# Performance work log

Hardware: AMD Instinct MI355X
Metric: run time of the kernel (lower is better)

Reference implementation:

```python
import jax, jax.numpy as jnp
import numpy as np

D_MODEL = 1024
N_HEAD = 16
D_HEAD = D_MODEL // N_HEAD
B, S = 4, 2048


def setup_inputs() -> dict:
    key = jax.random.key(0)
    ks = jax.random.split(key, 10)
    def xavier(k, shape):
        fan_in, fan_out = shape[1], shape[0]
        limit = np.sqrt(6.0 / (fan_in + fan_out))
        return jax.random.uniform(k, shape, jnp.float32, -limit, limit)
    x = jax.random.normal(ks[0], (B, S, D_MODEL), jnp.float32)
    mask = jnp.tril(jnp.ones((S, S), jnp.int32))[None, None]  # causal [1,1,S,S]
    return {
        "x": x,
        "Wq": xavier(ks[1], (D_MODEL, D_MODEL)), "bq": jnp.zeros((D_MODEL,), jnp.float32),
        "Wk": xavier(ks[2], (D_MODEL, D_MODEL)), "bk": jnp.zeros((D_MODEL,), jnp.float32),
        "Wv": xavier(ks[3], (D_MODEL, D_MODEL)), "bv": jnp.zeros((D_MODEL,), jnp.float32),
        "Wo": xavier(ks[4], (D_MODEL, D_MODEL)), "bo": jnp.zeros((D_MODEL,), jnp.float32),
        "mask": mask,
    }


def reference(x, Wq, bq, Wk, bk, Wv, bv, Wo, bo, mask):
    b, s, d = x.shape
    # Linear layers use y = x @ W.T + b (torch convention)
    def proj(W, bias):
        y = jnp.einsum('bsd,ed->bse', x, W) + bias
        return y.reshape(b, s, N_HEAD, D_HEAD).transpose(0, 2, 1, 3)  # [B,H,S,Dh]
    q = proj(Wq, bq)
    k = proj(Wk, bk)
    v = proj(Wv, bv)
    scores = jnp.einsum('bhqd,bhkd->bhqk', q, k) / jnp.sqrt(jnp.float32(D_HEAD))
    scores = jnp.where(mask == 0, jnp.float32(-1e9), scores)
    attn = jax.nn.softmax(scores, axis=-1)  # dropout is identity at eval
    context = jnp.einsum('bhqk,bhkd->bhqd', attn, v)
    context = context.transpose(0, 2, 1, 3).reshape(b, s, d)
    return jnp.einsum('bsd,ed->bse', context, Wo) + bo
```

## Files before the change

### kernel.cpp

```cpp
#include <hip/hip_runtime.h>
#include <stdint.h>

#define D_MODEL 1024
#define NHEAD   16
#define DHEAD   64
#define BATCH   4
#define SEQ     2048
#define MTOT    (BATCH*SEQ)

typedef __attribute__((ext_vector_type(4)))  float f32x4;
typedef __attribute__((ext_vector_type(8)))  short bf16x8;

typedef __attribute__((address_space(3))) uint32_t lds_u32;
typedef const __attribute__((address_space(1))) uint32_t glb_u32;

__device__ static inline void gload_lds16(const void* g, void* l) {
    __builtin_amdgcn_global_load_lds((glb_u32*)g, (lds_u32*)l, 16, 0, 0);
}

__device__ static inline ushort f2bf(float f) {
    uint32_t u = __builtin_bit_cast(uint32_t, f);
    u += 0x7fffu + ((u >> 16) & 1u);
    return (ushort)(u >> 16);
}

__device__ static inline float exp2_fast(float x) {
    float r; asm("v_exp_f32 %0, %1" : "=v"(r) : "v"(x)); return r;
}
__device__ static inline uint32_t cvt_pk_bf16(float a, float b) {
    uint32_t r;
    asm("v_cvt_pk_bf16_f32 %0, %1, %2" : "=v"(r) : "v"(a), "v"(b));
    return r;
}

__global__ __launch_bounds__(256) void convert_kernel(
    const float4* __restrict__ x,
    const float4* __restrict__ wq, const float4* __restrict__ wk,
    const float4* __restrict__ wv, const float4* __restrict__ wo,
    ushort4* __restrict__ xb, ushort4* __restrict__ wb)
{
    const int NX4 = (MTOT * D_MODEL) / 4;
    const int NW4 = (D_MODEL * D_MODEL) / 4;
    const int TOT = NX4 + 4 * NW4;
    for (int i = blockIdx.x * blockDim.x + threadIdx.x; i < TOT;
         i += gridDim.x * blockDim.x) {
        float4 v; ushort4* dst;
        if (i < NX4) { v = x[i]; dst = &xb[i]; }
        else {
            int j = i - NX4;
            int w = j >> 18;
            int r = j & (NW4 - 1);
            const float4* s = (w == 0) ? wq : (w == 1) ? wk : (w == 2) ? wv : wo;
            v = s[r]; dst = &wb[(size_t)w * NW4 + r];
        }
        ushort4 o;
        o.x = f2bf(v.x); o.y = f2bf(v.y); o.z = f2bf(v.z); o.w = f2bf(v.w);
        *dst = o;
    }
}


#define GEMM256_BODY(APTR, BPTR)                                            \
    __shared__ __align__(16) ushort S[2 * 32768];   \
    const int tid = threadIdx.x;                                            \
    const int w = tid >> 6, l = tid & 63;                                   \
    const int lo = l & 15, hi = l >> 4;                        \
    const int wm = w >> 2, wn = w & 3;                         \
    const int sr = l >> 3, sg = l & 7;                                      \
    f32x4 acc[8][4] = {};                                                   \
    auto stage = [&](int buf, int kt) {                                     \
        ushort* SP = &S[buf * 32768];                                       \
        _Pragma("unroll")                                                   \
        for (int j = 0; j < 4; ++j) {                                       \
            const int row = w * 32 + j * 8 + sr;                            \
            const int g = sg ^ sr;                         \
            gload_lds16((APTR) + (size_t)(m0 + row) * 1024 + kt * 64 + g * 8,\
                        SP + (w * 32 + j * 8) * 64);                        \
            gload_lds16((BPTR) + (size_t)(n0 + row) * 1024 + kt * 64 + g * 8,\
                        SP + 16384 + (w * 32 + j * 8) * 64);                \
        }                                                                   \
    };                                                                      \
    stage(0, 0);                                                            \
    asm volatile("s_waitcnt vmcnt(0)" ::: "memory");                        \
    __builtin_amdgcn_s_barrier();                                           \
    __builtin_amdgcn_sched_barrier(0);                                      \
    int cur = 0;                                                            \
    for (int kt = 0; kt < 16; ++kt) {                                       \
        if (kt + 1 < 16) stage(cur ^ 1, kt + 1);                            \
        const char* SA = (const char*)&S[cur * 32768];                      \
        const char* SB = SA + 32768;                                        \
        _Pragma("unroll")                                                   \
        for (int ks = 0; ks < 2; ++ks) {                                    \
            bf16x8 af[8], bfr[4];                                           \
            _Pragma("unroll")                                               \
            for (int mi = 0; mi < 8; ++mi) {                                \
                const int r = wm * 128 + mi * 16 + lo;                      \
                af[mi] = *(const bf16x8*)(SA + r * 128 +                    \
                          (((ks * 4 + hi) ^ (r & 7)) << 4));                \
            }                                                               \
            _Pragma("unroll")                                               \
            for (int ni = 0; ni < 4; ++ni) {                                \
                const int c = wn * 64 + ni * 16 + lo;                       \
                bfr[ni] = *(const bf16x8*)(SB + c * 128 +                   \
                          (((ks * 4 + hi) ^ (c & 7)) << 4));                \
            }                                                               \
            asm volatile("s_waitcnt lgkmcnt(0)" ::: "memory");              \
            __builtin_amdgcn_sched_barrier(0);                              \
            __builtin_amdgcn_s_setprio(1);                                  \
            _Pragma("unroll")                                               \
            for (int mi = 0; mi < 8; ++mi)                                  \
                _Pragma("unroll")                                           \
                for (int ni = 0; ni < 4; ++ni)                              \
                    acc[mi][ni] = __builtin_amdgcn_mfma_f32_16x16x32_bf16(  \
                        af[mi], bfr[ni], acc[mi][ni], 0, 0, 0);             \
            __builtin_amdgcn_s_setprio(0);                                  \
        }                                                                   \
        if (kt + 1 < 16) {                                                  \
            asm volatile("s_waitcnt vmcnt(0)" ::: "memory");                \
            __builtin_amdgcn_s_barrier();                                   \
            __builtin_amdgcn_sched_barrier(0);                              \
        }                                                                   \
        cur ^= 1;                                                           \
    }

__global__ __launch_bounds__(512) void gemm_qkv(
    const ushort* __restrict__ A,
    const ushort* __restrict__ W3,
    const float* __restrict__ bq, const float* __restrict__ bk,
    const float* __restrict__ bv,
    ushort* __restrict__ Qb, ushort* __restrict__ Kb, ushort* __restrict__ Vtb,
    float qscale)
{
    const int id = blockIdx.x;
    const int xcd = id & 7, q = id >> 3;
    const int mb = xcd * 4 + (q & 3);
    const int nb = q >> 2;
    const int m0 = mb * 256, n0 = nb * 256;

    GEMM256_BODY(A, W3)

    const int region = nb >> 2;
    const float scale = (region == 0) ? qscale : 1.0f;
    const float* bias = (region == 0) ? bq : (region == 1) ? bk : bv;
    ushort* outQK = (region == 0) ? Qb : Kb;

#pragma unroll
    for (int mi = 0; mi < 8; ++mi) {
#pragma unroll
        for (int ni = 0; ni < 4; ++ni) {
            const int gj  = n0 + wn * 64 + ni * 16 + lo;
            const int lcl = gj & 1023;
            const int h = lcl >> 6, dh = lcl & 63;
            const float bj = bias[lcl];
            const int gi0 = m0 + wm * 128 + mi * 16 + hi * 4;
            const int b = gi0 >> 11, s0 = gi0 & (SEQ - 1);
            if (region < 2) {
#pragma unroll
                for (int r = 0; r < 4; ++r)
                    outQK[(((size_t)(b * NHEAD + h)) * SEQ + s0 + r) * DHEAD + dh] =
                        f2bf((acc[mi][ni][r] + bj) * scale);
            } else {
                ushort4 o4;
                o4.x = f2bf(acc[mi][ni][0] + bj);
                o4.y = f2bf(acc[mi][ni][1] + bj);
                o4.z = f2bf(acc[mi][ni][2] + bj);
                o4.w = f2bf(acc[mi][ni][3] + bj);
                *(ushort4*)&Vtb[(((size_t)(b * NHEAD + h)) * DHEAD + dh) * SEQ + s0] = o4;
            }
        }
    }
}

__global__ __launch_bounds__(512) void gemm_out(
    const ushort* __restrict__ A,
    const ushort* __restrict__ W,
    const float*  __restrict__ bias,
    float* __restrict__ out)
{
    const int id = blockIdx.x;
    const int xcd = id & 7, q = id >> 3;
    const int mb = xcd * 4 + (q & 3);
    const int nb = q >> 2;
    const int m0 = mb * 256, n0 = nb * 256;

    GEMM256_BODY(A, W)

#pragma unroll
    for (int mi = 0; mi < 8; ++mi)
#pragma unroll
        for (int ni = 0; ni < 4; ++ni) {
            const int gj = n0 + wn * 64 + ni * 16 + lo;
            const float bj = bias[gj];
            const int gi0 = m0 + wm * 128 + mi * 16 + hi * 4;
#pragma unroll
            for (int r = 0; r < 4; ++r)
                out[(size_t)(gi0 + r) * D_MODEL + gj] = acc[mi][ni][r] + bj;
        }
}

__global__ __launch_bounds__(256) void attn_kernel(
    const ushort* __restrict__ Q, const ushort* __restrict__ K,
    const ushort* __restrict__ Vt, ushort* __restrict__ ctx)
{
    __shared__ __align__(16) ushort Ks[64 * 64];
    __shared__ __align__(16) ushort Vs[64 * 64];
    __shared__ __align__(16) ushort Pq[4 * 32 * 64];

    const int tid = threadIdx.x;
    const int w = tid >> 6, l = tid & 63, lo = l & 15, hi = l >> 4;
    const int sw = lo & 7;

    const int fid = blockIdx.x;
    const int xcd = fid & 7;
    const int g = xcd * 8 + ((fid >> 3) & 7);
    const int b = g >> 4, h = g & 15;
    const int j = (fid >> 6) & 7;
    const int half = fid >> 9;
    const int qt = half ? (15 - j) : j;
    const size_t base = (size_t)(b * NHEAD + h) * SEQ * DHEAD;

    const int krow = tid >> 3;
    const int kcol = (tid & 7) * 8;
    char* PqW = (char*)&Pq[w * 2048];

    const int q0 = qt << 7;
    const int qw0 = q0 + w * 32;

    bf16x8 qf[2][2];
#pragma unroll
    for (int mi = 0; mi < 2; ++mi)
#pragma unroll
        for (int ks = 0; ks < 2; ++ks)
            qf[mi][ks] = *(const bf16x8*)&Q[base +
                (size_t)(qw0 + mi * 16 + lo) * DHEAD + ks * 32 + hi * 8];

    f32x4 o[2][4] = {};
    float mrow[2] = {-1e30f, -1e30f}, lrow[2] = {0.f, 0.f};

    const int ntiles = (q0 + 128) >> 6;

    bf16x8 kregA[2], vregA[2], kregB[2], vregB[2];
#pragma unroll
    for (int c = 0; c < 2; ++c) {
        kregA[c] = *(const bf16x8*)&K[base + (size_t)(c * 32 + krow) * DHEAD + kcol];
        vregA[c] = *(const bf16x8*)&Vt[base + (size_t)(c * 32 + krow) * SEQ + kcol];
        kregB[c] = *(const bf16x8*)&K[base + (size_t)(64 + c * 32 + krow) * DHEAD + kcol];
        vregB[c] = *(const bf16x8*)&Vt[base + (size_t)(c * 32 + krow) * SEQ + 64 + kcol];
    }

    auto tile_body = [&](int t, bf16x8 (&KR)[2], bf16x8 (&VR)[2]) {
        const int kv0 = t << 6;
        __syncthreads();
#pragma unroll
        for (int c = 0; c < 2; ++c) {
            const int row = c * 32 + krow;
            const int g16 = (tid & 7) ^ (row & 7);
            *(bf16x8*)((char*)Ks + row * 128 + (g16 << 4)) = KR[c];
            *(bf16x8*)((char*)Vs + row * 128 + (g16 << 4)) = VR[c];
        }
        __syncthreads();
        if (t + 2 < ntiles) {
            const int nv0 = kv0 + 128;
#pragma unroll
            for (int c = 0; c < 2; ++c) {
                KR[c] = *(const bf16x8*)&K[base + (size_t)(nv0 + c * 32 + krow) * DHEAD + kcol];
                VR[c] = *(const bf16x8*)&Vt[base + (size_t)(c * 32 + krow) * SEQ + nv0 + kcol];
            }
        }
        if (kv0 > qw0 + 31) return;

        f32x4 s[2][4] = {};
        __builtin_amdgcn_s_setprio(1);
#pragma unroll
        for (int ks = 0; ks < 2; ++ks) {
            bf16x8 kf[4];
#pragma unroll
            for (int nj = 0; nj < 4; ++nj)
                kf[nj] = *(const bf16x8*)((char*)Ks + (nj * 16 + lo) * 128 +
                                          ((((ks << 2) + hi) ^ sw) << 4));
#pragma unroll
            for (int mi = 0; mi < 2; ++mi)
#pragma unroll
                for (int nj = 0; nj < 4; ++nj)
                    s[mi][nj] = __builtin_amdgcn_mfma_f32_16x16x32_bf16(
                        kf[nj], qf[mi][ks], s[mi][nj], 0, 0, 0);
        }
        __builtin_amdgcn_s_setprio(0);

        if (kv0 + 63 > qw0) {
#pragma unroll
            for (int mi = 0; mi < 2; ++mi) {
                const int gq = qw0 + mi * 16 + lo;
#pragma unroll
                for (int nj = 0; nj < 4; ++nj)
#pragma unroll
                    for (int r = 0; r < 4; ++r) {
                        const int gk = kv0 + nj * 16 + hi * 4 + r;
                        if (gk > gq) s[mi][nj][r] = -1e30f;
                    }
            }
        }

        float tl[2], corr[2];
#pragma unroll
        for (int mi = 0; mi < 2; ++mi) {
            float m = s[mi][0][0];
#pragma unroll
            for (int nj = 0; nj < 4; ++nj)
#pragma unroll
                for (int r = 0; r < 4; ++r) m = fmaxf(m, s[mi][nj][r]);
            tl[mi] = m;
        }
        const bool grow = (tl[0] > mrow[0] + 8.f) | (tl[1] > mrow[1] + 8.f);
        if (__any(grow)) {
#pragma unroll
            for (int mi = 0; mi < 2; ++mi) {
                float m2 = fmaxf(tl[mi], __shfl_xor(tl[mi], 16));
                m2 = fmaxf(m2, __shfl_xor(m2, 32));
                const float mn = fmaxf(mrow[mi], m2);
                corr[mi] = exp2_fast(mrow[mi] - mn);
                mrow[mi] = mn;
            }
#pragma unroll
            for (int mi = 0; mi < 2; ++mi)
#pragma unroll
                for (int r = 0; r < 4; ++r) {
                    const float cb = __shfl(corr[mi], hi * 4 + r);
#pragma unroll
                    for (int ni = 0; ni < 4; ++ni) o[mi][ni][r] *= cb;
                }
        } else { corr[0] = 1.f; corr[1] = 1.f; }

#pragma unroll
        for (int mi = 0; mi < 2; ++mi) {
            float ls = 0.f;
#pragma unroll
            for (int nj = 0; nj < 4; ++nj) {
#pragma unroll
                for (int r = 0; r < 4; ++r) {
                    const float p = exp2_fast(s[mi][nj][r] - mrow[mi]);
                    s[mi][nj][r] = p;
                    ls += p;
                }
                uint2 pp;
                pp.x = cvt_pk_bf16(s[mi][nj][0], s[mi][nj][1]);
                pp.y = cvt_pk_bf16(s[mi][nj][2], s[mi][nj][3]);
                const int gP = ((nj << 1) + (hi >> 1)) ^ sw;
                *(uint2*)(PqW + (mi * 16 + lo) * 128 + (gP << 4) + ((hi & 1) << 3)) = pp;
            }
            ls += __shfl_xor(ls, 16);
            ls += __shfl_xor(ls, 32);
            lrow[mi] = lrow[mi] * corr[mi] + ls;
        }

        __builtin_amdgcn_s_setprio(1);
#pragma unroll
        for (int ks2 = 0; ks2 < 2; ++ks2) {
            bf16x8 pf[2], vf[4];
#pragma unroll
            for (int mi = 0; mi < 2; ++mi)
                pf[mi] = *(const bf16x8*)(PqW + (mi * 16 + lo) * 128 +
                                          ((((ks2 << 2) + hi) ^ sw) << 4));
#pragma unroll
            for (int ni = 0; ni < 4; ++ni)
                vf[ni] = *(const bf16x8*)((char*)Vs + (ni * 16 + lo) * 128 +
                                          ((((ks2 << 2) + hi) ^ sw) << 4));
#pragma unroll
            for (int mi = 0; mi < 2; ++mi)
#pragma unroll
                for (int ni = 0; ni < 4; ++ni)
                    o[mi][ni] = __builtin_amdgcn_mfma_f32_16x16x32_bf16(
                        pf[mi], vf[ni], o[mi][ni], 0, 0, 0);
        }
        __builtin_amdgcn_s_setprio(0);
    };

    for (int tt = 0; tt < ntiles; tt += 2) {
        tile_body(tt,     kregA, vregA);
        tile_body(tt + 1, kregB, vregB);
    }

#pragma unroll
    for (int mi = 0; mi < 2; ++mi) {
        const float rv = 1.0f / lrow[mi];
#pragma unroll
        for (int r = 0; r < 4; ++r) {
            const float rb = __shfl(rv, hi * 4 + r);
            const int gq = qw0 + mi * 16 + hi * 4 + r;
#pragma unroll
            for (int ni = 0; ni < 4; ++ni)
                ctx[((size_t)(b * SEQ + gq)) * D_MODEL + h * DHEAD + ni * 16 + lo] =
                    f2bf(o[mi][ni][r] * rb);
        }
    }
}

extern "C" void kernel_launch(void* const* d_in, const int* in_sizes, int n_in,
                              void* d_out, int out_size, void* d_ws, size_t ws_size,
                              hipStream_t stream) {
    const float* x  = (const float*)d_in[0];
    const float* Wq = (const float*)d_in[1];
    const float* bq = (const float*)d_in[2];
    const float* Wk = (const float*)d_in[3];
    const float* bk = (const float*)d_in[4];
    const float* Wv = (const float*)d_in[5];
    const float* bv = (const float*)d_in[6];
    const float* Wo = (const float*)d_in[7];
    const float* bo = (const float*)d_in[8];

    char* ws = (char*)d_ws;
    ushort* xb  = (ushort*)(ws);
    ushort* wb  = (ushort*)(ws + (16u << 20));
    ushort* Qb  = (ushort*)(ws + (24u << 20));
    ushort* Kb  = (ushort*)(ws + (40u << 20));
    ushort* Vtb = (ushort*)(ws + (56u << 20));
    ushort* ctx = (ushort*)(ws + (72u << 20));

    convert_kernel<<<2048, 256, 0, stream>>>(
        (const float4*)x, (const float4*)Wq, (const float4*)Wk,
        (const float4*)Wv, (const float4*)Wo, (ushort4*)xb, (ushort4*)wb);

    const int NW = D_MODEL * D_MODEL;
    const float qscale = 0.125f * 1.44269504f;

    gemm_qkv<<<384, 512, 0, stream>>>(xb, wb, bq, bk, bv, Qb, Kb, Vtb, qscale);

    attn_kernel<<<1024, 256, 0, stream>>>(Qb, Kb, Vtb, ctx);

    gemm_out<<<128, 512, 0, stream>>>(ctx, wb + 3 * NW, bo, (float*)d_out);
}
```

Baseline: 171.0 us.

## Load GEMM B operand directly to registers, stage only A through LDS

```diff
diff --git a/kernel.cpp b/kernel.cpp
--- a/kernel.cpp
+++ b/kernel.cpp
@@ -61,66 +61,75 @@
 
 
 #define GEMM256_BODY(APTR, BPTR)                                            \
-    __shared__ __align__(16) ushort S[2 * 32768];   \
+    __shared__ __align__(16) ushort S[2 * 16384];      \
     const int tid = threadIdx.x;                                            \
     const int w = tid >> 6, l = tid & 63;                                   \
     const int lo = l & 15, hi = l >> 4;                        \
     const int wm = w >> 2, wn = w & 3;                         \
-    const int sr = l >> 3, sg = l & 7;                                      \
+    const int sr = w * 8 + (l >> 3), sg = l & 7;                            \
     f32x4 acc[8][4] = {};                                                   \
-    auto stage = [&](int buf, int kt) {                                     \
-        ushort* SP = &S[buf * 32768];                                       \
+    auto stageA = [&](int buf, int kt) {                                    \
+        ushort* SP = &S[buf * 16384];                                       \
         _Pragma("unroll")                                                   \
         for (int j = 0; j < 4; ++j) {                                       \
-            const int row = w * 32 + j * 8 + sr;                            \
-            const int g = sg ^ sr;                         \
+            const int row = j * 64 + sr;                                    \
+            const int g = sg ^ (row & 7);                                   \
             gload_lds16((APTR) + (size_t)(m0 + row) * 1024 + kt * 64 + g * 8,\
-                        SP + (w * 32 + j * 8) * 64);                        \
-            gload_lds16((BPTR) + (size_t)(n0 + row) * 1024 + kt * 64 + g * 8,\
-                        SP + 16384 + (w * 32 + j * 8) * 64);                \
+                        SP + (j * 64 + w * 8) * 64);                        \
         }                                                                   \
     };                                                                      \
-    stage(0, 0);                                                            \
+    const ushort* Bb = (BPTR) + (size_t)(n0 + wn * 64 + lo) * 1024 + hi * 8;\
+    auto loadB = [&](bf16x8 (&B)[8], int kt) {                              \
+        _Pragma("unroll")                                                   \
+        for (int ni = 0; ni < 4; ++ni)                                      \
+            _Pragma("unroll")                                               \
+            for (int ks = 0; ks < 2; ++ks)                                  \
+                B[ni * 2 + ks] = *(const bf16x8*)(Bb +                      \
+                    (size_t)(ni * 16) * 1024 + kt * 64 + ks * 32);          \
+    };                                                                      \
+    bf16x8 B0[8], B1[8];                                                    \
+    loadB(B0, 0);                                                           \
+    stageA(0, 0);                                                           \
     asm volatile("s_waitcnt vmcnt(0)" ::: "memory");                        \
     __builtin_amdgcn_s_barrier();                                           \
     __builtin_amdgcn_sched_barrier(0);                                      \
-    int cur = 0;                                                            \
-    for (int kt = 0; kt < 16; ++kt) {                                       \
-        if (kt + 1 < 16) stage(cur ^ 1, kt + 1);                            \
-        const char* SA = (const char*)&S[cur * 32768];                      \
-        const char* SB = SA + 32768;                                        \
+    auto ktStep = [&](int kt, int buf, bf16x8 (&Bc)[8], bf16x8 (&Bn)[8]) {  \
+        if (kt + 1 < 16) { stageA(buf ^ 1, kt + 1); loadB(Bn, kt + 1); }    \
+        const char* SA = (const char*)&S[buf * 16384];                      \
         _Pragma("unroll")                                                   \
         for (int ks = 0; ks < 2; ++ks) {                                    \
-            bf16x8 af[8], bfr[4];                                           \
             _Pragma("unroll")                                               \
-            for (int mi = 0; mi < 8; ++mi) {                                \
-                const int r = wm * 128 + mi * 16 + lo;                      \
-                af[mi] = *(const bf16x8*)(SA + r * 128 +                    \
-                          (((ks * 4 + hi) ^ (r & 7)) << 4));                \
+            for (int half = 0; half < 2; ++half) {                          \
+                bf16x8 af[4];                                               \
+                _Pragma("unroll")                                           \
+                for (int mi = 0; mi < 4; ++mi) {                            \
+                    const int r = wm * 128 + (half * 4 + mi) * 16 + lo;     \
+                    af[mi] = *(const bf16x8*)(SA + r * 128 +                \
+                              (((ks * 4 + hi) ^ (r & 7)) << 4));            \
+                }                                                           \
+                asm volatile("s_waitcnt lgkmcnt(0)" ::: "memory");          \
+                __builtin_amdgcn_sched_barrier(0);                          \
+                __builtin_amdgcn_s_setprio(1);                              \
+                _Pragma("unroll")                                           \
+                for (int mi = 0; mi < 4; ++mi)                              \
+                    _Pragma("unroll")                                       \
+                    for (int ni = 0; ni < 4; ++ni)                          \
+                        acc[half * 4 + mi][ni] =                            \
+                            __builtin_amdgcn_mfma_f32_16x16x32_bf16(        \
+                                af[mi], Bc[ni * 2 + ks],                    \
+                                acc[half * 4 + mi][ni], 0, 0, 0);           \
+                __builtin_amdgcn_s_setprio(0);                              \
             }                                                               \
-            _Pragma("unroll")                                               \
-            for (int ni = 0; ni < 4; ++ni) {                                \
-                const int c = wn * 64 + ni * 16 + lo;                       \
-                bfr[ni] = *(const bf16x8*)(SB + c * 128 +                   \
-                          (((ks * 4 + hi) ^ (c & 7)) << 4));                \
-            }                                                               \
-            asm volatile("s_waitcnt lgkmcnt(0)" ::: "memory");              \
-            __builtin_amdgcn_sched_barrier(0);                              \
-            __builtin_amdgcn_s_setprio(1);                                  \
-            _Pragma("unroll")                                               \
-            for (int mi = 0; mi < 8; ++mi)                                  \
-                _Pragma("unroll")                                           \
-                for (int ni = 0; ni < 4; ++ni)                              \
-                    acc[mi][ni] = __builtin_amdgcn_mfma_f32_16x16x32_bf16(  \
-                        af[mi], bfr[ni], acc[mi][ni], 0, 0, 0);             \
-            __builtin_amdgcn_s_setprio(0);                                  \
         }                                                                   \
         if (kt + 1 < 16) {                                                  \
             asm volatile("s_waitcnt vmcnt(0)" ::: "memory");                \
             __builtin_amdgcn_s_barrier();                                   \
             __builtin_amdgcn_sched_barrier(0);                              \
         }                                                                   \
-        cur ^= 1;                                                           \
+    };                                                                      \
+    for (int t = 0; t < 16; t += 2) {                                       \
+        ktStep(t,     0, B0, B1);                                           \
+        ktStep(t + 1, 1, B1, B0);                                           \
     }
 
 __global__ __launch_bounds__(512) void gemm_qkv(
```

After: 345.6 us. 2.02x slower.
